# Kernel optimization log

Hardware: AMD Instinct MI355X
Metric: run time of the kernel (lower is better)

Reference implementation:

```python
import jax, jax.numpy as jnp
import numpy as np

L, B, C, H = 1024, 8, 1024, 16
D = C // H  # 64


def setup_inputs() -> dict:
    key = jax.random.key(0)
    ks = jax.random.split(key, 8)
    hidden_states = jax.random.normal(ks[0], (L, B, C), dtype=jnp.float32)
    rotary_pos_emb = jax.random.uniform(ks[1], (L, D // 2), dtype=jnp.float32) * 10.0
    attention_mask = jax.random.randint(ks[2], (B, L, L), 0, 2) > 0
    s = 1.0 / np.sqrt(C)
    Wqkv = jax.random.uniform(ks[3], (3 * C, C), dtype=jnp.float32, minval=-s, maxval=s)
    bqkv = jax.random.uniform(ks[4], (3 * C,), dtype=jnp.float32, minval=-s, maxval=s)
    Wo = jax.random.uniform(ks[5], (C, C), dtype=jnp.float32, minval=-s, maxval=s)
    bo = jax.random.uniform(ks[6], (C,), dtype=jnp.float32, minval=-s, maxval=s)
    return {"hidden_states": hidden_states, "rotary_pos_emb": rotary_pos_emb,
            "attention_mask": attention_mask, "Wqkv": Wqkv, "bqkv": bqkv, "Wo": Wo, "bo": bo}


def _rotate_half(x):
    # interleaved pairs: [-x1, x0, -x3, x2, ...]
    x2 = x.reshape(*x.shape[:-1], -1, 2)
    return jnp.stack((-x2[..., 1], x2[..., 0]), axis=-1).reshape(x.shape)


def reference(hidden_states, rotary_pos_emb, attention_mask, Wqkv, bqkv, Wo, bo):
    Lx, Bx, Cx = hidden_states.shape
    # QKV projection: (L,B,3C) -> (3,B,L,H,D)
    qkv = hidden_states @ Wqkv.T + bqkv
    qkv = qkv.reshape(Lx, Bx, 3, H, D).transpose(2, 1, 0, 3, 4)
    q, k, v = qkv[0], qkv[1], qkv[2]  # (B, L, H, D)
    # RoPE: freqs (L, D/2) -> cos/sin (1, L, 1, D) via duplication
    rpe = rotary_pos_emb[None] if rotary_pos_emb.ndim == 2 else rotary_pos_emb
    cos = jnp.concatenate([jnp.cos(rpe), jnp.cos(rpe)], axis=-1)[:, :, None, :]
    sin = jnp.concatenate([jnp.sin(rpe), jnp.sin(rpe)], axis=-1)[:, :, None, :]
    q = q * cos + _rotate_half(q) * sin
    k = k * cos + _rotate_half(k) * sin
    # (B, H, L, D)
    q = q.transpose(0, 2, 1, 3)
    k = k.transpose(0, 2, 1, 3)
    v = v.transpose(0, 2, 1, 3)
    scale = 1.0 / jnp.sqrt(jnp.asarray(D, dtype=q.dtype))
    scores = jnp.einsum('bhqd,bhkd->bhqk', q, k) * scale
    # torch SDPA bool mask: True = attend, False = masked
    scores = jnp.where(attention_mask[:, None, :, :], scores, jnp.finfo(scores.dtype).min)
    attn = jax.nn.softmax(scores, axis=-1)
    out = jnp.einsum('bhqk,bhkd->bhqd', attn, v)  # (B, H, L, D)
    out = out.transpose(2, 0, 1, 3).reshape(Lx, Bx, Cx)  # (L, B, C)
    return out @ Wo.T + bo
```

## Files before the change

kernel.cpp:

```cpp
#include <hip/hip_runtime.h>
#include <hip/hip_bf16.h>

typedef short bf16x8 __attribute__((ext_vector_type(8)));
typedef short bf16x4 __attribute__((ext_vector_type(4)));
typedef float f32x4 __attribute__((ext_vector_type(4)));
typedef unsigned int u32;
typedef unsigned long long u64;

#define GLD_LDS16(gp, lp) \
  __builtin_amdgcn_global_load_lds((const __attribute__((address_space(1))) u32*)(gp), \
                                   (__attribute__((address_space(3))) u32*)(lp), 16, 0, 0)

__device__ __forceinline__ short f2bf(float f) {
  u32 u = __builtin_bit_cast(u32, f);
  u = (u + 0x7fffu + ((u >> 16) & 1u)) >> 16;
  return (short)u;
}

__device__ __forceinline__ u32 pack2_bf16(float a, float b) {
#if __has_builtin(__builtin_amdgcn_cvt_pk_bf16_f32)
  typedef __bf16 bf16v2 __attribute__((ext_vector_type(2)));
  bf16v2 r = __builtin_amdgcn_cvt_pk_bf16_f32(a, b);
  return __builtin_bit_cast(u32, r);
#else
  u32 r;
  asm("v_cvt_pk_bf16_f32 %0, %1, %2" : "=v"(r) : "v"(a), "v"(b));
  return r;
#endif
}

__device__ __forceinline__ float exp2_fast(float x) {
#if __has_builtin(__builtin_amdgcn_exp2f)
  return __builtin_amdgcn_exp2f(x);
#else
  return exp2f(x);
#endif
}


__global__ __launch_bounds__(256) void cvt_all(
    const float* __restrict__ hs, const float* __restrict__ wqkv,
    const float* __restrict__ wo, short* __restrict__ xb,
    short* __restrict__ wqkvb, short* __restrict__ wob) {
  int b = blockIdx.x;
  const float* in;
  short* out;
  int base;
  if (b < 8192) {
    in = hs; out = xb; base = b * 1024;
  } else if (b < 8192 + 3072) {
    in = wqkv; out = wqkvb; base = (b - 8192) * 1024;
  } else {
    in = wo; out = wob; base = (b - 11264) * 1024;
  }
  int i = base + threadIdx.x * 4;
  float4 v = *(const float4*)(in + i);
  short4 o;
  o.x = f2bf(v.x); o.y = f2bf(v.y); o.z = f2bf(v.z); o.w = f2bf(v.w);
  *(short4*)(out + i) = o;
}

__global__ void rope_tables(const float* __restrict__ rpe, float* __restrict__ cosT,
                            float* __restrict__ sinT) {
  int i = blockIdx.x * 256 + threadIdx.x;
  float v = rpe[i];
  cosT[i] = cosf(v);
  sinT[i] = sinf(v);
}

__global__ void mask_pack(const int* __restrict__ m, u64* __restrict__ out) {
  int i = blockIdx.x * 256 + threadIdx.x;
  u64 bm = __ballot(m[i] != 0);
  if ((threadIdx.x & 63) == 0) out[i >> 6] = bm;
}

__global__ __launch_bounds__(256, 2) void gemm_qkv(
    const short* __restrict__ Xb, const short* __restrict__ Wb,
    const float* __restrict__ bqkv, const float* __restrict__ cosT,
    const float* __restrict__ sinT, short* __restrict__ qb,
    short* __restrict__ kbuf, short* __restrict__ vbuf) {
  __shared__ short Ash[128 * 32];
  __shared__ short Bsh[128 * 32];
  const int tid = threadIdx.x;
  const int wid = tid >> 6, lane = tid & 63;
  const int g = lane >> 4, c = lane & 15;
  const int wm = wid >> 1, wn = wid & 1;
  const int m0 = blockIdx.y * 128, n0 = blockIdx.x * 128;

  f32x4 acc[4][4];
  for (int i = 0; i < 4; i++)
    for (int j = 0; j < 4; j++) acc[i][j] = (f32x4){0.f, 0.f, 0.f, 0.f};

  const int srow = lane >> 2;
  const int scol = (lane & 3) * 8;
  const short* AgL = Xb + (long)(m0 + wid * 32 + srow) * 1024 + scol;
  const short* BgL = Wb + (long)(n0 + wid * 32 + srow) * 1024 + scol;
  short* As0 = &Ash[(wid * 32) * 32];
  short* As1 = &Ash[(wid * 32 + 16) * 32];
  short* Bs0 = &Bsh[(wid * 32) * 32];
  short* Bs1 = &Bsh[(wid * 32 + 16) * 32];

  for (int kt = 0; kt < 32; ++kt) {
    const int ko = kt * 32;
    GLD_LDS16(AgL + ko, As0);
    GLD_LDS16(AgL + ko + 16 * 1024, As1);
    GLD_LDS16(BgL + ko, Bs0);
    GLD_LDS16(BgL + ko + 16 * 1024, Bs1);
    __syncthreads();
    bf16x8 af[4], bfr[4];
    for (int i = 0; i < 4; i++)
      af[i] = *(const bf16x8*)&Ash[(wm * 64 + i * 16 + c) * 32 + g * 8];
    for (int j = 0; j < 4; j++)
      bfr[j] = *(const bf16x8*)&Bsh[(wn * 64 + j * 16 + c) * 32 + g * 8];
    for (int i = 0; i < 4; i++)
      for (int j = 0; j < 4; j++)
        acc[i][j] = __builtin_amdgcn_mfma_f32_16x16x32_bf16(bfr[j], af[i], acc[i][j], 0, 0, 0);
    __syncthreads();
  }

  for (int jt = 0; jt < 4; jt++) {
    const int chan = n0 + wn * 64 + jt * 16 + g * 4;
    const int three = chan >> 10;
    const int hh = (chan >> 6) & 15;
    const int d = chan & 63;
    const float4 bq = *(const float4*)&bqkv[chan];
    for (int i = 0; i < 4; i++) {
      const int r = m0 + wm * 64 + i * 16 + c;
      const int l = r >> 3, b = r & 7;
      float v0 = acc[i][jt][0] + bq.x;
      float v1 = acc[i][jt][1] + bq.y;
      float v2 = acc[i][jt][2] + bq.z;
      float v3 = acc[i][jt][3] + bq.w;
      const long doff = ((long)(b * 16 + hh) * 1024 + l) * 64 + d;
      if (three == 2) {
        uint2 o = {pack2_bf16(v0, v1), pack2_bf16(v2, v3)};
        *(uint2*)&vbuf[doff] = o;
      } else {
        const float4 cs = *(const float4*)&cosT[l * 32 + (d & 31)];
        const float4 sn = *(const float4*)&sinT[l * 32 + (d & 31)];
        float e0 = v0 * cs.x - v1 * sn.x;
        float o0 = v1 * cs.y + v0 * sn.y;
        float e1 = v2 * cs.z - v3 * sn.z;
        float o1 = v3 * cs.w + v2 * sn.w;
        short* dst;
        if (three == 0) {
          const float S = 0.18033688011f;
          e0 *= S; o0 *= S; e1 *= S; o1 *= S;
          dst = qb;
        } else {
          dst = kbuf;
        }
        uint2 o = {pack2_bf16(e0, o0), pack2_bf16(e1, o1)};
        *(uint2*)&dst[doff] = o;
      }
    }
  }
}

__global__ __launch_bounds__(256) void transpose_v(const short* __restrict__ vbuf,
                                                   short* __restrict__ vTb) {
  __shared__ short T[64 * 72];
  const int bh = blockIdx.y;
  const int l0 = blockIdx.x * 64;
  const int t = threadIdx.x;
  const int row = t >> 3;
  const int cc = (t & 7) * 8;
  const short* src = vbuf + ((long)bh * 1024 + l0) * 64;
  for (int p = 0; p < 2; p++) {
    int lr = row + p * 32;
    *(bf16x8*)&T[lr * 72 + cc] = *(const bf16x8*)&src[(long)lr * 64 + cc];
  }
  __syncthreads();
  short* dst = vTb + (long)bh * 64 * 1024 + l0;
  for (int p = 0; p < 2; p++) {
    int d = row + p * 32;
    bf16x8 v;
    for (int j = 0; j < 8; j++) v[j] = T[(cc + j) * 72 + d];
    *(bf16x8*)&dst[(long)d * 1024 + cc] = v;
  }
}

__global__ __launch_bounds__(256, 5) void flash_attn(
    const short* __restrict__ qb, const short* __restrict__ kbuf,
    const short* __restrict__ vTb, const u64* __restrict__ maskb,
    short* __restrict__ attno) {
  __shared__ short K0[64 * 64], K1[64 * 64];
  __shared__ short V0[64 * 64], V1[64 * 64];
  const int t = threadIdx.x;
  const int wid = t >> 6, lane = t & 63;
  const int g = lane >> 4, c = lane & 15;
  const int q0 = blockIdx.x * 64;
  const int bh = blockIdx.y;
  const int b = bh >> 4;
  const int h = bh & 15;
  const long qoff = (long)bh * 1024 * 64;
  const int qrow = q0 + wid * 16 + c;

  bf16x8 aq0, aq1;
  {
    const short* qp = qb + qoff + (long)qrow * 64;
    aq0 = *(const bf16x8*)(qp + g * 8);
    aq1 = *(const bf16x8*)(qp + 32 + g * 8);
  }

  f32x4 Od[4];
  for (int i = 0; i < 4; i++) Od[i] = (f32x4){0.f, 0.f, 0.f, 0.f};
  f32x4 Ld = (f32x4){0.f, 0.f, 0.f, 0.f};
  float m_run = -1e30f;

  bf16x8 avOnes8;
  {
    union { bf16x8 v; u32 u[4]; } av;
    u32 o1 = (c == 0) ? 0x3F803F80u : 0u;
    av.u[0] = av.u[1] = av.u[2] = av.u[3] = o1;
    avOnes8 = av.v;
  }

  const u64* mrow = maskb + ((long)b * 1024 + qrow) * 16;
  const short* Kg = kbuf + qoff;
  const short* Vg = vTb + qoff;

  const int l8 = lane >> 3, l7 = lane & 7;
  const int sr = wid * 16 + l8;
  const int sch = ((l7 ^ l8) & 7) * 8;
  const int r1 = wid * 16 + l8;
  const int r2 = r1 + 8;
  const int kp1 = (r1 & 32) | (((r1 & 15) >> 2) << 3) | (((r1 >> 4) & 1) << 2) | (r1 & 3);
  const int kp2 = (r2 & 32) | (((r2 & 15) >> 2) << 3) | (((r2 >> 4) & 1) << 2) | (r2 & 3);

  const int ck0 = g ^ (c & 7);
  const int kOff0 = c * 64 + ck0 * 8;
  const int kOff1 = c * 64 + (ck0 ^ 4) * 8;
  int vOff32[2];
  for (int kg = 0; kg < 2; kg++)
    vOff32[kg] = c * 64 + (((kg * 4 + g) ^ (c & 7)) * 8);

#define STAGE(KD, VD, ktn) do { \
    GLD_LDS16(Kg + (long)((ktn) + kp1) * 64 + sch,      &KD[(wid * 16) * 64]); \
    GLD_LDS16(Kg + (long)((ktn) + kp2) * 64 + sch,      &KD[(wid * 16 + 8) * 64]); \
    GLD_LDS16(Vg + (long)sr * 1024 + (ktn) + sch,       &VD[(wid * 16) * 64]); \
    GLD_LDS16(Vg + (long)(sr + 8) * 1024 + (ktn) + sch, &VD[(wid * 16 + 8) * 64]); \
  } while (0)

#define TILE(KB, VB, KP, VP, ki) do { \
    u64 mw = mrow[ki];  \
    __syncthreads();  \
    STAGE(KP, VP, (((ki) + 1) & 15) * 64); \
    f32x4 z[4]; \
    for (int nt = 0; nt < 4; nt++) { \
      bf16x8 bk0 = *(const bf16x8*)&KB[kOff0 + nt * 1024]; \
      bf16x8 bk1 = *(const bf16x8*)&KB[kOff1 + nt * 1024]; \
      f32x4 zz = (f32x4){0.f, 0.f, 0.f, 0.f}; \
      zz = __builtin_amdgcn_mfma_f32_16x16x32_bf16(bk0, aq0, zz, 0, 0, 0); \
      zz = __builtin_amdgcn_mfma_f32_16x16x32_bf16(bk1, aq1, zz, 0, 0, 0); \
      z[nt] = zz; \
    } \
    float mx = fmaxf(fmaxf(fmaxf(z[0][0], z[0][1]), fmaxf(z[0][2], z[0][3])), \
                     fmaxf(fmaxf(z[1][0], z[1][1]), fmaxf(z[1][2], z[1][3]))); \
    mx = fmaxf(mx, fmaxf(fmaxf(fmaxf(z[2][0], z[2][1]), fmaxf(z[2][2], z[2][3])), \
                         fmaxf(fmaxf(z[3][0], z[3][1]), fmaxf(z[3][2], z[3][3])))); \
    if (__ballot(mx > m_run + 8.f)) {  \
      mx = fmaxf(mx, __shfl_xor(mx, 16, 64)); \
      mx = fmaxf(mx, __shfl_xor(mx, 32, 64)); \
      float mnew = fmaxf(m_run, mx); \
      float al = exp2_fast(m_run - mnew); \
      for (int dt = 0; dt < 4; dt++) { \
        Od[dt][0] *= al; Od[dt][1] *= al; Od[dt][2] *= al; Od[dt][3] *= al; \
      } \
      Ld[0] *= al; \
      m_run = mnew; \
    } \
    for (int kg = 0; kg < 2; kg++) { \
      union { bf16x8 v; u32 u[4]; } pu; \
      for (int ntp = 0; ntp < 2; ntp++) { \
        const int nt = kg * 2 + ntp; \
        u32 m4 = (u32)(mw >> (kg * 32 + g * 8 + ntp * 4)) & 0xFu; \
        u32 mlo = ((m4 & 1u) ? 0xFFFFu : 0u) | ((m4 & 2u) ? 0xFFFF0000u : 0u); \
        u32 mhi = ((m4 & 4u) ? 0xFFFFu : 0u) | ((m4 & 8u) ? 0xFFFF0000u : 0u); \
        float p0 = exp2_fast(z[nt][0] - m_run); \
        float p1 = exp2_fast(z[nt][1] - m_run); \
        float p2 = exp2_fast(z[nt][2] - m_run); \
        float p3 = exp2_fast(z[nt][3] - m_run); \
        pu.u[ntp * 2 + 0] = pack2_bf16(p0, p1) & mlo; \
        pu.u[ntp * 2 + 1] = pack2_bf16(p2, p3) & mhi; \
      } \
      Ld = __builtin_amdgcn_mfma_f32_16x16x32_bf16(avOnes8, pu.v, Ld, 0, 0, 0); \
      for (int dt = 0; dt < 4; dt++) { \
        bf16x8 av = *(const bf16x8*)&VB[vOff32[kg] + dt * 1024]; \
        Od[dt] = __builtin_amdgcn_mfma_f32_16x16x32_bf16(av, pu.v, Od[dt], 0, 0, 0); \
      } \
    } \
  } while (0)

  STAGE(K0, V0, 0);
  for (int ki = 0; ki < 16; ki += 2) {
    TILE(K0, V0, K1, V1, ki);
    TILE(K1, V1, K0, V0, ki + 1);
  }
#undef TILE
#undef STAGE

  float lsum = __shfl(Ld[0], c, 64);
  float inv = 1.f / lsum;
  long rbase = ((long)qrow * 8 + b) * 1024 + h * 64 + g * 4;
  for (int dt = 0; dt < 4; dt++) {
    union { bf16x4 v; u32 u[2]; } o;
    o.u[0] = pack2_bf16(Od[dt][0] * inv, Od[dt][1] * inv);
    o.u[1] = pack2_bf16(Od[dt][2] * inv, Od[dt][3] * inv);
    *(bf16x4*)&attno[rbase + dt * 16] = o.v;
  }
}

__global__ __launch_bounds__(256, 2) void gemm_out(
    const short* __restrict__ Ab, const short* __restrict__ Wob,
    const float* __restrict__ bo, float* __restrict__ out) {
  __shared__ short Ash[128 * 32];
  __shared__ short Bsh[128 * 32];
  const int tid = threadIdx.x;
  const int wid = tid >> 6, lane = tid & 63;
  const int g = lane >> 4, c = lane & 15;
  const int wm = wid >> 1, wn = wid & 1;
  const int m0 = blockIdx.y * 128, n0 = blockIdx.x * 128;

  f32x4 acc[4][4];
  for (int i = 0; i < 4; i++)
    for (int j = 0; j < 4; j++) acc[i][j] = (f32x4){0.f, 0.f, 0.f, 0.f};

  const int srow = lane >> 2;
  const int scol = (lane & 3) * 8;
  const short* AgL = Ab + (long)(m0 + wid * 32 + srow) * 1024 + scol;
  const short* BgL = Wob + (long)(n0 + wid * 32 + srow) * 1024 + scol;
  short* As0 = &Ash[(wid * 32) * 32];
  short* As1 = &Ash[(wid * 32 + 16) * 32];
  short* Bs0 = &Bsh[(wid * 32) * 32];
  short* Bs1 = &Bsh[(wid * 32 + 16) * 32];

  for (int kt = 0; kt < 32; ++kt) {
    const int ko = kt * 32;
    GLD_LDS16(AgL + ko, As0);
    GLD_LDS16(AgL + ko + 16 * 1024, As1);
    GLD_LDS16(BgL + ko, Bs0);
    GLD_LDS16(BgL + ko + 16 * 1024, Bs1);
    __syncthreads();
    bf16x8 af[4], bfr[4];
    for (int i = 0; i < 4; i++)
      af[i] = *(const bf16x8*)&Ash[(wm * 64 + i * 16 + c) * 32 + g * 8];
    for (int j = 0; j < 4; j++)
      bfr[j] = *(const bf16x8*)&Bsh[(wn * 64 + j * 16 + c) * 32 + g * 8];
    for (int i = 0; i < 4; i++)
      for (int j = 0; j < 4; j++)
        acc[i][j] = __builtin_amdgcn_mfma_f32_16x16x32_bf16(af[i], bfr[j], acc[i][j], 0, 0, 0);
    __syncthreads();
  }

  for (int jt = 0; jt < 4; jt++) {
    const int j = n0 + wn * 64 + jt * 16 + c;
    const float bias = bo[j];
    for (int i = 0; i < 4; i++) {
      const int rbase = m0 + wm * 64 + i * 16 + g * 4;
      for (int reg = 0; reg < 4; reg++)
        out[(long)(rbase + reg) * 1024 + j] = acc[i][jt][reg] + bias;
    }
  }
}

extern "C" void kernel_launch(void* const* d_in, const int* in_sizes, int n_in,
                              void* d_out, int out_size, void* d_ws, size_t ws_size,
                              hipStream_t stream) {
  const float* hs = (const float*)d_in[0];
  const float* rpe = (const float*)d_in[1];
  const int* amask = (const int*)d_in[2];
  const float* Wqkv = (const float*)d_in[3];
  const float* bqkv = (const float*)d_in[4];
  const float* Wo = (const float*)d_in[5];
  const float* bo = (const float*)d_in[6];
  float* out = (float*)d_out;

  char* ws = (char*)d_ws;
  auto alloc = [&](size_t bytes) {
    char* p = ws;
    ws += (bytes + 255) & ~(size_t)255;
    return p;
  };
  short* Xb = (short*)alloc(8192LL * 1024 * 2);
  short* Wqkvb = (short*)alloc(3072LL * 1024 * 2);
  short* Wob = (short*)alloc(1024LL * 1024 * 2);
  float* cosT = (float*)alloc(1024 * 32 * 4);
  float* sinT = (float*)alloc(1024 * 32 * 4);
  u64* maskb = (u64*)alloc(8LL * 1024 * 16 * 8);
  short* qb = (short*)alloc(128LL * 1024 * 64 * 2);
  short* kbuf = (short*)alloc(128LL * 1024 * 64 * 2);
  short* vbuf = (short*)alloc(128LL * 1024 * 64 * 2);
  short* vTb = (short*)alloc(128LL * 1024 * 64 * 2);
  short* attno = (short*)alloc(8192LL * 1024 * 2);

  cvt_all<<<12288, 256, 0, stream>>>(hs, Wqkv, Wo, Xb, Wqkvb, Wob);
  rope_tables<<<128, 256, 0, stream>>>(rpe, cosT, sinT);
  mask_pack<<<32768, 256, 0, stream>>>(amask, maskb);
  gemm_qkv<<<dim3(24, 64), 256, 0, stream>>>(Xb, Wqkvb, bqkv, cosT, sinT, qb, kbuf, vbuf);
  transpose_v<<<dim3(16, 128), 256, 0, stream>>>(vbuf, vTb);
  flash_attn<<<dim3(16, 128), 256, 0, stream>>>(qb, kbuf, vTb, maskb, attno);
  gemm_out<<<dim3(8, 64), 256, 0, stream>>>(attno, Wob, bo, out);
}
```

Baseline: 329.1 us.

## Double-buffer LDS with XOR swizzle in QKV and output projection GEMMs

Both projection GEMMs now keep two LDS stages, issuing the next K-tile's global-to-LDS loads before computing on the current tile and waiting only on the older loads with vmcnt. The global column offset is XOR-swizzled with the row, and the fragment reads apply the matching swizzle, to reduce LDS bank conflicts on the bf16x8 reads. Launch bounds go from 2 to 4 blocks per SM to allow higher occupancy. The cost is double the LDS footprint, plus one wasted wrap-around prefetch on the final iteration.

```diff
diff --git a/kernel.cpp b/kernel.cpp
--- a/kernel.cpp
+++ b/kernel.cpp
@@ -74,13 +74,13 @@
   if ((threadIdx.x & 63) == 0) out[i >> 6] = bm;
 }
 
-__global__ __launch_bounds__(256, 2) void gemm_qkv(
+__global__ __launch_bounds__(256, 4) void gemm_qkv(
     const short* __restrict__ Xb, const short* __restrict__ Wb,
     const float* __restrict__ bqkv, const float* __restrict__ cosT,
     const float* __restrict__ sinT, short* __restrict__ qb,
     short* __restrict__ kbuf, short* __restrict__ vbuf) {
-  __shared__ short Ash[128 * 32];
-  __shared__ short Bsh[128 * 32];
+  __shared__ short Ash[2][128 * 32];
+  __shared__ short Bsh[2][128 * 32];
   const int tid = threadIdx.x;
   const int wid = tid >> 6, lane = tid & 63;
   const int g = lane >> 4, c = lane & 15;
@@ -92,31 +92,42 @@
     for (int j = 0; j < 4; j++) acc[i][j] = (f32x4){0.f, 0.f, 0.f, 0.f};
 
   const int srow = lane >> 2;
-  const int scol = (lane & 3) * 8;
+  const int scol = ((lane & 3) ^ ((lane >> 3) & 3)) * 8;
   const short* AgL = Xb + (long)(m0 + wid * 32 + srow) * 1024 + scol;
   const short* BgL = Wb + (long)(n0 + wid * 32 + srow) * 1024 + scol;
-  short* As0 = &Ash[(wid * 32) * 32];
-  short* As1 = &Ash[(wid * 32 + 16) * 32];
-  short* Bs0 = &Bsh[(wid * 32) * 32];
-  short* Bs1 = &Bsh[(wid * 32 + 16) * 32];
-
-  for (int kt = 0; kt < 32; ++kt) {
-    const int ko = kt * 32;
-    GLD_LDS16(AgL + ko, As0);
-    GLD_LDS16(AgL + ko + 16 * 1024, As1);
-    GLD_LDS16(BgL + ko, Bs0);
-    GLD_LDS16(BgL + ko + 16 * 1024, Bs1);
-    __syncthreads();
-    bf16x8 af[4], bfr[4];
-    for (int i = 0; i < 4; i++)
-      af[i] = *(const bf16x8*)&Ash[(wm * 64 + i * 16 + c) * 32 + g * 8];
-    for (int j = 0; j < 4; j++)
-      bfr[j] = *(const bf16x8*)&Bsh[(wn * 64 + j * 16 + c) * 32 + g * 8];
-    for (int i = 0; i < 4; i++)
-      for (int j = 0; j < 4; j++)
-        acc[i][j] = __builtin_amdgcn_mfma_f32_16x16x32_bf16(bfr[j], af[i], acc[i][j], 0, 0, 0);
-    __syncthreads();
-  }
+  const int dst0 = (wid * 32) * 32;
+  const int dst1 = (wid * 32 + 16) * 32;
+  const int ck = g ^ ((c >> 1) & 3);
+
+#define QKV_KSTEP(CA, CB, PA, PB, nko) do { \
+    GLD_LDS16(AgL + (nko), &(PA)[dst0]); \
+    GLD_LDS16(AgL + (nko) + 16 * 1024, &(PA)[dst1]); \
+    GLD_LDS16(BgL + (nko), &(PB)[dst0]); \
+    GLD_LDS16(BgL + (nko) + 16 * 1024, &(PB)[dst1]); \
+    asm volatile("s_waitcnt vmcnt(4)" ::: "memory"); \
+    __builtin_amdgcn_s_barrier(); \
+    __builtin_amdgcn_sched_barrier(0); \
+    bf16x8 af[4], bfr[4]; \
+    for (int i = 0; i < 4; i++) \
+      af[i] = *(const bf16x8*)&(CA)[(wm * 64 + i * 16 + c) * 32 + ck * 8]; \
+    for (int j = 0; j < 4; j++) \
+      bfr[j] = *(const bf16x8*)&(CB)[(wn * 64 + j * 16 + c) * 32 + ck * 8]; \
+    for (int i = 0; i < 4; i++) \
+      for (int j = 0; j < 4; j++) \
+        acc[i][j] = __builtin_amdgcn_mfma_f32_16x16x32_bf16(bfr[j], af[i], acc[i][j], 0, 0, 0); \
+    __builtin_amdgcn_sched_barrier(0); \
+    __builtin_amdgcn_s_barrier(); \
+  } while (0)
+
+  GLD_LDS16(AgL, &Ash[0][dst0]);
+  GLD_LDS16(AgL + 16 * 1024, &Ash[0][dst1]);
+  GLD_LDS16(BgL, &Bsh[0][dst0]);
+  GLD_LDS16(BgL + 16 * 1024, &Bsh[0][dst1]);
+  for (int kt = 0; kt < 32; kt += 2) {
+    QKV_KSTEP(Ash[0], Bsh[0], Ash[1], Bsh[1], (kt + 1) * 32);
+    QKV_KSTEP(Ash[1], Bsh[1], Ash[0], Bsh[0], ((kt + 2) & 31) * 32);
+  }
+#undef QKV_KSTEP
 
   for (int jt = 0; jt < 4; jt++) {
     const int chan = n0 + wn * 64 + jt * 16 + g * 4;
@@ -311,11 +322,11 @@
   }
 }
 
-__global__ __launch_bounds__(256, 2) void gemm_out(
+__global__ __launch_bounds__(256, 4) void gemm_out(
     const short* __restrict__ Ab, const short* __restrict__ Wob,
     const float* __restrict__ bo, float* __restrict__ out) {
-  __shared__ short Ash[128 * 32];
-  __shared__ short Bsh[128 * 32];
+  __shared__ short Ash[2][128 * 32];
+  __shared__ short Bsh[2][128 * 32];
   const int tid = threadIdx.x;
   const int wid = tid >> 6, lane = tid & 63;
   const int g = lane >> 4, c = lane & 15;
@@ -327,31 +338,42 @@
     for (int j = 0; j < 4; j++) acc[i][j] = (f32x4){0.f, 0.f, 0.f, 0.f};
 
   const int srow = lane >> 2;
-  const int scol = (lane & 3) * 8;
+  const int scol = ((lane & 3) ^ ((lane >> 3) & 3)) * 8;
   const short* AgL = Ab + (long)(m0 + wid * 32 + srow) * 1024 + scol;
   const short* BgL = Wob + (long)(n0 + wid * 32 + srow) * 1024 + scol;
-  short* As0 = &Ash[(wid * 32) * 32];
-  short* As1 = &Ash[(wid * 32 + 16) * 32];
-  short* Bs0 = &Bsh[(wid * 32) * 32];
-  short* Bs1 = &Bsh[(wid * 32 + 16) * 32];
-
-  for (int kt = 0; kt < 32; ++kt) {
-    const int ko = kt * 32;
-    GLD_LDS16(AgL + ko, As0);
-    GLD_LDS16(AgL + ko + 16 * 1024, As1);
-    GLD_LDS16(BgL + ko, Bs0);
-    GLD_LDS16(BgL + ko + 16 * 1024, Bs1);
-    __syncthreads();
-    bf16x8 af[4], bfr[4];
-    for (int i = 0; i < 4; i++)
-      af[i] = *(const bf16x8*)&Ash[(wm * 64 + i * 16 + c) * 32 + g * 8];
-    for (int j = 0; j < 4; j++)
-      bfr[j] = *(const bf16x8*)&Bsh[(wn * 64 + j * 16 + c) * 32 + g * 8];
-    for (int i = 0; i < 4; i++)
-      for (int j = 0; j < 4; j++)
-        acc[i][j] = __builtin_amdgcn_mfma_f32_16x16x32_bf16(af[i], bfr[j], acc[i][j], 0, 0, 0);
-    __syncthreads();
-  }
+  const int dst0 = (wid * 32) * 32;
+  const int dst1 = (wid * 32 + 16) * 32;
+  const int ck = g ^ ((c >> 1) & 3);
+
+#define OUT_KSTEP(CA, CB, PA, PB, nko) do { \
+    GLD_LDS16(AgL + (nko), &(PA)[dst0]); \
+    GLD_LDS16(AgL + (nko) + 16 * 1024, &(PA)[dst1]); \
+    GLD_LDS16(BgL + (nko), &(PB)[dst0]); \
+    GLD_LDS16(BgL + (nko) + 16 * 1024, &(PB)[dst1]); \
+    asm volatile("s_waitcnt vmcnt(4)" ::: "memory"); \
+    __builtin_amdgcn_s_barrier(); \
+    __builtin_amdgcn_sched_barrier(0); \
+    bf16x8 af[4], bfr[4]; \
+    for (int i = 0; i < 4; i++) \
+      af[i] = *(const bf16x8*)&(CA)[(wm * 64 + i * 16 + c) * 32 + ck * 8]; \
+    for (int j = 0; j < 4; j++) \
+      bfr[j] = *(const bf16x8*)&(CB)[(wn * 64 + j * 16 + c) * 32 + ck * 8]; \
+    for (int i = 0; i < 4; i++) \
+      for (int j = 0; j < 4; j++) \
+        acc[i][j] = __builtin_amdgcn_mfma_f32_16x16x32_bf16(af[i], bfr[j], acc[i][j], 0, 0, 0); \
+    __builtin_amdgcn_sched_barrier(0); \
+    __builtin_amdgcn_s_barrier(); \
+  } while (0)
+
+  GLD_LDS16(AgL, &Ash[0][dst0]);
+  GLD_LDS16(AgL + 16 * 1024, &Ash[0][dst1]);
+  GLD_LDS16(BgL, &Bsh[0][dst0]);
+  GLD_LDS16(BgL + 16 * 1024, &Bsh[0][dst1]);
+  for (int kt = 0; kt < 32; kt += 2) {
+    OUT_KSTEP(Ash[0], Bsh[0], Ash[1], Bsh[1], (kt + 1) * 32);
+    OUT_KSTEP(Ash[1], Bsh[1], Ash[0], Bsh[0], ((kt + 2) & 31) * 32);
+  }
+#undef OUT_KSTEP
 
   for (int jt = 0; jt < 4; jt++) {
     const int j = n0 + wn * 64 + jt * 16 + c;
```

Result: no change. 326.4 us (-0.8%).
